# Performance work log

Measured on AMD Instinct MI355X. Metric: run time of the kernel, lower is better.

Reference implementation:

```python
import jax, jax.numpy as jnp
import numpy as np

# Dims and constants
B, DIN, H = 32768, 256, 256
STEPS = 3                 # ode_steps (>1 -> RK2 branch)
DT = 1.0 / STEPS
TAU_MIN = 0.2
ALPHA = 0.1               # plastic (hebb) mixing coefficient
ETA = 0.1                 # hebb learning rate
DECAY = 0.99              # hebb trace decay
MOE_WEIGHT = 1.0


def setup_inputs() -> dict:
    key = jax.random.key(0)
    ks = jax.random.split(key, 8)
    s = 0.02
    return {
        "x": jax.random.normal(ks[0], (B, DIN), dtype=jnp.float32),
        "h": jax.random.normal(ks[1], (B, H), dtype=jnp.float32),
        "hebb_ih": jnp.zeros((DIN, H), dtype=jnp.float32),
        "hebb_hh": jnp.zeros((H, H), dtype=jnp.float32),
        # PlasticSynapse base weights (torch Linear layout [out, in])
        "W_ih": jax.random.normal(ks[2], (H, DIN), dtype=jnp.float32) * s,
        "b_ih": jnp.zeros((H,), dtype=jnp.float32),
        "W_hh": jax.random.normal(ks[3], (H, H), dtype=jnp.float32) * s,
        "b_hh": jnp.zeros((H,), dtype=jnp.float32),
        # tau_net: Linear(DIN+H -> H) -> SiLU -> Linear(H -> H) -> Softplus
        "W_t1": jax.random.normal(ks[4], (H, DIN + H), dtype=jnp.float32) * s,
        "b_t1": jnp.zeros((H,), dtype=jnp.float32),
        "W_t2": jax.random.normal(ks[5], (H, H), dtype=jnp.float32) * s,
        "b_t2": jnp.zeros((H,), dtype=jnp.float32),
    }


def reference(x, h, hebb_ih, hebb_hh, W_ih, b_ih, W_hh, b_hh, W_t1, b_t1, W_t2, b_t2):
    bsz = x.shape[0]
    step_moe = MOE_WEIGHT / STEPS

    def syn(inp, W, b, hebb):
        # PlasticSynapse: fixed weight + alpha-scaled Hebbian trace
        return inp @ (W.T + ALPHA * hebb) + b

    def tau_net(hh):
        z = jnp.concatenate([x, hh], axis=-1)          # [B, DIN+H]
        u = z @ W_t1.T + b_t1
        u = u * jax.nn.sigmoid(u)                      # SiLU
        return jax.nn.softplus(u @ W_t2.T + b_t2) + TAU_MIN

    def dynamics(hh, heb_ih, heb_hh):
        interaction = jnp.tanh(syn(x, W_ih, b_ih, heb_ih) + syn(hh, W_hh, b_hh, heb_hh))
        return (-hh + interaction) / tau_net(hh)

    def update_hebb(hebb, pre, post):
        # decayed trace + batch-mean outer product, scaled by per-step moe weight
        return DECAY * hebb + (ETA * step_moe / bsz) * (pre.T @ post)

    # RK2 loop (steps = 3, fixed) with mid-point Hebbian updates, per original forward
    for _ in range(STEPS):
        k1 = dynamics(h, hebb_ih, hebb_hh)
        h_mid = h + 0.5 * DT * k1
        hebb_ih = update_hebb(hebb_ih, x, h_mid)
        hebb_hh = update_hebb(hebb_hh, h_mid, h_mid)
        k2 = dynamics(h_mid, hebb_ih, hebb_hh)
        h = h + DT * k2
    return h
```

## Files before the change

kernel.cpp:

```cpp
#include <hip/hip_runtime.h>
#include <stdint.h>

typedef unsigned short u16;
typedef short v8s __attribute__((ext_vector_type(8)));
typedef short v4s __attribute__((ext_vector_type(4)));
typedef float v4f __attribute__((ext_vector_type(4)));

#define NB 32768
#define ND 256
#define DTF (1.0f/3.0f)
#define ALPHA 0.1f
#define DECAY 0.99f
#define TAU_MIN 0.2f
#define HEBB_SCALE (0.1f*(1.0f/3.0f)/32768.0f)

__device__ __forceinline__ float b2f(u16 h){ return __uint_as_float(((unsigned)h)<<16); }
__device__ __forceinline__ u16 f2b(float f){
  unsigned u = __float_as_uint(f);
  u += 0x7FFFu + ((u>>16)&1u);
  return (u16)(u>>16);
}

__global__ void k_copy(const float* __restrict__ x, const float* __restrict__ h,
                       u16* __restrict__ x_bf, float* __restrict__ h_state){
  const long tot = (long)NB*ND/4;
  for (long i = blockIdx.x*(long)blockDim.x + threadIdx.x; i < tot;
       i += (long)gridDim.x*blockDim.x){
    v4f xv = *(const v4f*)(x + 4*i);
    u16 t4[4];
#pragma unroll
    for (int e=0;e<4;++e) t4[e] = f2b(xv[e]);
    *(v4s*)(x_bf + 4*i) = *(v4s*)t4;
    *(v4f*)(h_state + 4*i) = *(const v4f*)(h + 4*i);
  }
}

__global__ void k_transpose_x(const float* __restrict__ x, u16* __restrict__ xT){
  __shared__ u16 ld[64*65];
  int bt = blockIdx.x >> 2, it = blockIdx.x & 3;
  long b0 = (long)bt*64; int i0 = it*64;
  int t = threadIdx.x;
#pragma unroll
  for (int e=0;e<16;++e){
    int idx = e*256 + t; int r = idx>>6, c = idx&63;
    ld[c + r*65] = f2b(x[(b0+r)*ND + i0 + c]);
  }
  __syncthreads();
#pragma unroll
  for (int e=0;e<16;++e){
    int idx = e*256 + t; int rr = idx>>6, cc = idx&63;
    xT[(long)(i0+rr)*NB + b0 + cc] = ld[cc*65 + rr];
  }
}

__global__ void k_prep_w(const float* __restrict__ W_ih, const float* __restrict__ W_hh,
                         const float* __restrict__ W_t1, const float* __restrict__ W_t2,
                         const float* __restrict__ hebb_ih, const float* __restrict__ hebb_hh,
                         u16* __restrict__ weff_ih, u16* __restrict__ weff_hh,
                         u16* __restrict__ wt1a, u16* __restrict__ wt1b, u16* __restrict__ wt2){
  int i = blockIdx.x*blockDim.x + threadIdx.x;
  if (i >= ND*ND) return;
  int n = i >> 8, k = i & 255;
  weff_ih[i] = f2b(W_ih[i] + ALPHA*hebb_ih[k*ND + n]);
  weff_hh[i] = f2b(W_hh[i] + ALPHA*hebb_hh[k*ND + n]);
  wt1a[i] = f2b(W_t1[n*512 + k]);
  wt1b[i] = f2b(W_t1[n*512 + 256 + k]);
  wt2[i]  = f2b(W_t2[i]);
}

__launch_bounds__(512,2)
__global__ void k_gemmP(const u16* __restrict__ x_bf, const u16* __restrict__ wt1a,
                        const float* __restrict__ b_t1, u16* __restrict__ P){
  __shared__ u16 lA[128*40];
  __shared__ u16 lB[256*40];
  int t = threadIdx.x, lid = t&63, wid = t>>6, wm = wid>>2, wn = wid&3, lr = lid&15, lg = lid>>4;
  long row0 = (long)blockIdx.x*128;
  v4f z = {0.f,0.f,0.f,0.f};
  v4f acc[4][4];
#pragma unroll
  for (int a=0;a<4;++a)
#pragma unroll
    for (int b=0;b<4;++b) acc[a][b] = z;
  for (int c=0; c<8; ++c){
    __syncthreads();
    { int r=t>>2, sg=t&3;
      *(v8s*)&lA[r*40+sg*8] = *(const v8s*)(x_bf + (row0+r)*ND + c*32 + sg*8); }
#pragma unroll
    for (int it2=0; it2<2; ++it2){
      int s2=t+it2*512; int n=s2>>2, sg=s2&3;
      *(v8s*)&lB[n*40+sg*8] = *(const v8s*)(wt1a + n*ND + c*32 + sg*8);
    }
    __syncthreads();
    v8s a[4], b[4];
#pragma unroll
    for (int mf=0;mf<4;++mf) a[mf] = *(v8s*)&lA[(wm*64+mf*16+lr)*40 + lg*8];
#pragma unroll
    for (int nf=0;nf<4;++nf) b[nf] = *(v8s*)&lB[(wn*64+nf*16+lr)*40 + lg*8];
#pragma unroll
    for (int mf=0;mf<4;++mf)
#pragma unroll
      for (int nf=0;nf<4;++nf)
        acc[mf][nf] = __builtin_amdgcn_mfma_f32_16x16x32_bf16(a[mf], b[nf], acc[mf][nf], 0,0,0);
  }
#pragma unroll
  for (int mf=0;mf<4;++mf)
#pragma unroll
    for (int nf=0;nf<4;++nf)
#pragma unroll
      for (int r=0;r<4;++r){
        int rr = wm*64+mf*16+lg*4+r, cc = wn*64+nf*16+lr;
        P[(row0+rr)*ND + cc] = f2b(acc[mf][nf][r] + b_t1[cc]);
      }
}

__launch_bounds__(512,2)
__global__ void k_dyn(const u16* __restrict__ x_bf, const float* __restrict__ evalF,
                      const float* __restrict__ baseF,
                      const u16* __restrict__ weff_ih, const u16* __restrict__ weff_hh,
                      const u16* __restrict__ wt1b, const u16* __restrict__ wt2,
                      const u16* __restrict__ P,
                      const float* __restrict__ b_ih, const float* __restrict__ b_hh,
                      const float* __restrict__ b_t2,
                      float coef, float* __restrict__ outF, u16* __restrict__ outT, int writeT){
  __shared__ u16 lA[128*40];
  __shared__ u16 lB[256*40];
  __shared__ u16 lU[35840];
  __shared__ float sb1[256];
  __shared__ float sb2[256];
  int t = threadIdx.x, lid = t&63, wid = t>>6, wm = wid>>2, wn = wid&3, lr = lid&15, lg = lid>>4;
  long row0 = (long)blockIdx.x*128;
  if (t < 256){ sb1[t] = b_ih[t] + b_hh[t]; sb2[t] = b_t2[t]; }
  v4f z = {0.f,0.f,0.f,0.f};
  v4f accI[4][4], acc2[4][4];
#pragma unroll
  for (int a=0;a<4;++a)
#pragma unroll
    for (int b=0;b<4;++b){ accI[a][b] = z; acc2[a][b] = z; }

  for (int c=0; c<16; ++c){
    __syncthreads();
    { int r=t>>2, sg=t&3;
      if (c < 8){
        *(v8s*)&lA[r*40+sg*8] = *(const v8s*)(x_bf + (row0+r)*ND + c*32 + sg*8);
      } else {
        const float* s = evalF + (row0+r)*ND + (c-8)*32 + sg*8;
        v4f v0 = *(const v4f*)s, v1 = *(const v4f*)(s+4);
        u16 tmp[8];
#pragma unroll
        for (int e=0;e<4;++e){ tmp[e]=f2b(v0[e]); tmp[4+e]=f2b(v1[e]); }
        *(v8s*)&lA[r*40+sg*8] = *(v8s*)tmp;
      }
    }
    const u16* W = (c<8) ? weff_ih : weff_hh;
    int ck = (c & 7)*32;
#pragma unroll
    for (int it2=0; it2<2; ++it2){
      int s2=t+it2*512; int n=s2>>2, sg=s2&3;
      *(v8s*)&lB[n*40+sg*8] = *(const v8s*)(W + n*ND + ck + sg*8);
    }
    __syncthreads();
    v8s a[4], b[4];
#pragma unroll
    for (int mf=0;mf<4;++mf) a[mf] = *(v8s*)&lA[(wm*64+mf*16+lr)*40 + lg*8];
#pragma unroll
    for (int nf=0;nf<4;++nf) b[nf] = *(v8s*)&lB[(wn*64+nf*16+lr)*40 + lg*8];
#pragma unroll
    for (int mf=0;mf<4;++mf)
#pragma unroll
      for (int nf=0;nf<4;++nf)
        accI[mf][nf] = __builtin_amdgcn_mfma_f32_16x16x32_bf16(a[mf], b[nf], accI[mf][nf], 0,0,0);
  }

  for (int c=0; c<8; ++c){
    __syncthreads();
    { int r=t>>2, sg=t&3;
      const float* s = evalF + (row0+r)*ND + c*32 + sg*8;
      v4f v0 = *(const v4f*)s, v1 = *(const v4f*)(s+4);
      u16 tmp[8];
#pragma unroll
      for (int e=0;e<4;++e){ tmp[e]=f2b(v0[e]); tmp[4+e]=f2b(v1[e]); }
      *(v8s*)&lA[r*40+sg*8] = *(v8s*)tmp;
    }
#pragma unroll
    for (int it2=0; it2<2; ++it2){
      int s2=t+it2*512; int n=s2>>2, sg=s2&3;
      *(v8s*)&lB[n*40+sg*8] = *(const v8s*)(wt1b + n*ND + c*32 + sg*8);
    }
    __syncthreads();
    v8s a[4], b[4];
#pragma unroll
    for (int mf=0;mf<4;++mf) a[mf] = *(v8s*)&lA[(wm*64+mf*16+lr)*40 + lg*8];
#pragma unroll
    for (int nf=0;nf<4;++nf) b[nf] = *(v8s*)&lB[(wn*64+nf*16+lr)*40 + lg*8];
#pragma unroll
    for (int mf=0;mf<4;++mf)
#pragma unroll
      for (int nf=0;nf<4;++nf)
        acc2[mf][nf] = __builtin_amdgcn_mfma_f32_16x16x32_bf16(a[mf], b[nf], acc2[mf][nf], 0,0,0);
  }

#pragma unroll
  for (int mf=0;mf<4;++mf)
#pragma unroll
    for (int nf=0;nf<4;++nf)
#pragma unroll
      for (int r=0;r<4;++r){
        int rr = wm*64+mf*16+lg*4+r, cc = wn*64+nf*16+lr;
        float v = acc2[mf][nf][r] + b2f(P[(row0+rr)*ND + cc]);
        float sgm = 1.f/(1.f + __expf(-v));
        lU[rr*280 + cc] = f2b(v*sgm);
      }

  v4f acc4[4][4];
#pragma unroll
  for (int a=0;a<4;++a)
#pragma unroll
    for (int b=0;b<4;++b) acc4[a][b] = z;
  for (int c=0; c<8; ++c){
    __syncthreads();
#pragma unroll
    for (int it2=0; it2<2; ++it2){
      int s2=t+it2*512; int n=s2>>2, sg=s2&3;
      *(v8s*)&lB[n*40+sg*8] = *(const v8s*)(wt2 + n*ND + c*32 + sg*8);
    }
    __syncthreads();
    v8s a[4], b[4];
#pragma unroll
    for (int mf=0;mf<4;++mf) a[mf] = *(v8s*)&lU[(wm*64+mf*16+lr)*280 + c*32 + lg*8];
#pragma unroll
    for (int nf=0;nf<4;++nf) b[nf] = *(v8s*)&lB[(wn*64+nf*16+lr)*40 + lg*8];
#pragma unroll
    for (int mf=0;mf<4;++mf)
#pragma unroll
      for (int nf=0;nf<4;++nf)
        acc4[mf][nf] = __builtin_amdgcn_mfma_f32_16x16x32_bf16(a[mf], b[nf], acc4[mf][nf], 0,0,0);
  }

  __syncthreads();
#pragma unroll
  for (int mf=0;mf<4;++mf)
#pragma unroll
    for (int nf=0;nf<4;++nf)
#pragma unroll
      for (int r=0;r<4;++r){
        int rr = wm*64+mf*16+lg*4+r, cc = wn*64+nf*16+lr;
        long gi = (row0+rr)*ND + cc;
        float pre = accI[mf][nf][r] + sb1[cc];
        float pc = fminf(fmaxf(pre, -15.f), 15.f);
        float e2 = __expf(2.f*pc);
        float inter = (e2 - 1.f)/(e2 + 1.f);
        float zz = acc4[mf][nf][r] + sb2[cc];
        float sp = (zz > 15.f) ? zz : __logf(1.f + __expf(zz));
        float tau = sp + TAU_MIN;
        float ev = evalF[gi];
        float o = baseF[gi] + coef*(inter - ev)/tau;
        outF[gi] = o;
        if (writeT) lU[cc*136 + rr] = f2b(o);
      }
  if (writeT){
    __syncthreads();
    int cc = t>>1, r0 = (t&1)*64;
#pragma unroll
    for (int e=0;e<8;++e){
      v8s v = *(v8s*)&lU[cc*136 + r0 + e*8];
      *(v8s*)(outT + (long)cc*NB + row0 + r0 + e*8) = v;
    }
  }
}

__launch_bounds__(512,2)
__global__ void k_hebb_part(const u16* __restrict__ xT, const u16* __restrict__ hmT,
                            u16* __restrict__ part){
  __shared__ u16 lA[256*40];
  __shared__ u16 lB[256*40];
  int t = threadIdx.x, lid = t&63, wid = t>>6, wm = wid>>2, wn = wid&3, lr = lid&15, lg = lid>>4;
  int mat = blockIdx.x & 1, chunk = blockIdx.x >> 1;
  const u16* Asrc = mat ? hmT : xT;
  v4f z = {0.f,0.f,0.f,0.f};
  v4f acc[8][4];
#pragma unroll
  for (int a=0;a<8;++a)
#pragma unroll
    for (int b=0;b<4;++b) acc[a][b] = z;
  for (int kc=0; kc<8; ++kc){
    long b0 = (long)chunk*256 + kc*32;
    __syncthreads();
#pragma unroll
    for (int it2=0; it2<2; ++it2){
      int s = t + it2*512; int rr = s>>2, sg = s&3;
      *(v8s*)&lA[rr*40+sg*8] = *(const v8s*)(Asrc + (long)rr*NB + b0 + sg*8);
      *(v8s*)&lB[rr*40+sg*8] = *(const v8s*)(hmT  + (long)rr*NB + b0 + sg*8);
    }
    __syncthreads();
    v8s a[8], b[4];
#pragma unroll
    for (int mf=0;mf<8;++mf) a[mf] = *(v8s*)&lA[(wm*128+mf*16+lr)*40 + lg*8];
#pragma unroll
    for (int nf=0;nf<4;++nf) b[nf] = *(v8s*)&lB[(wn*64+nf*16+lr)*40 + lg*8];
#pragma unroll
    for (int mf=0;mf<8;++mf)
#pragma unroll
      for (int nf=0;nf<4;++nf)
        acc[mf][nf] = __builtin_amdgcn_mfma_f32_16x16x32_bf16(a[mf], b[nf], acc[mf][nf], 0,0,0);
  }
  u16* dst = part + (long)blockIdx.x*65536;
#pragma unroll
  for (int mf=0;mf<8;++mf)
#pragma unroll
    for (int nf=0;nf<4;++nf)
#pragma unroll
      for (int r=0;r<4;++r){
        int i = wm*128+mf*16+lg*4+r, j = wn*64+nf*16+lr;
        dst[i*ND + j] = f2b(acc[mf][nf][r]);
      }
}

__global__ void k_hebb_reduce(const u16* __restrict__ part,
                              const float* __restrict__ prev_ih, const float* __restrict__ prev_hh,
                              float* __restrict__ next_ih, float* __restrict__ next_hh,
                              const float* __restrict__ W_ih, const float* __restrict__ W_hh,
                              u16* __restrict__ weff_ih, u16* __restrict__ weff_hh){
  int tid = blockIdx.x*blockDim.x + threadIdx.x;
  if (tid >= 2*ND*ND) return;
  int mat = tid >> 16;
  int rem = tid & 65535;
  float s = 0.f;
  for (int c=0; c<128; ++c) s += b2f(part[(long)((c<<1)+mat)*65536 + rem]);
  const float* prev = mat ? prev_hh : prev_ih;
  float nv = DECAY*prev[rem] + HEBB_SCALE*s;
  if (mat) next_hh[rem] = nv; else next_ih[rem] = nv;
  int k = rem >> 8, n = rem & 255;
  const float* Wb = mat ? W_hh : W_ih;
  u16 wv = f2b(Wb[n*ND + k] + ALPHA*nv);
  if (mat) weff_hh[n*ND + k] = wv; else weff_ih[n*ND + k] = wv;
}

extern "C" void kernel_launch(void* const* d_in, const int* in_sizes, int n_in,
                              void* d_out, int out_size, void* d_ws, size_t ws_size,
                              hipStream_t stream) {
  const float* x       = (const float*)d_in[0];
  const float* h       = (const float*)d_in[1];
  const float* hebb_ih = (const float*)d_in[2];
  const float* hebb_hh = (const float*)d_in[3];
  const float* W_ih    = (const float*)d_in[4];
  const float* b_ih    = (const float*)d_in[5];
  const float* W_hh    = (const float*)d_in[6];
  const float* b_hh    = (const float*)d_in[7];
  const float* W_t1    = (const float*)d_in[8];
  const float* b_t1    = (const float*)d_in[9];
  const float* W_t2    = (const float*)d_in[10];
  const float* b_t2    = (const float*)d_in[11];
  float* h_state = (float*)d_out;

  char* w = (char*)d_ws;
  u16* x_bf = (u16*)w;  w += 16777216;
  u16* xT   = (u16*)w;  w += 16777216;
  u16* P    = (u16*)w;  w += 16777216;
  u16* hmT  = (u16*)w;  w += 16777216;
  float* hmF = (float*)w; w += 33554432;
  u16* part = (u16*)w;  w += 33554432;
  float* hebA_ih = (float*)w; w += 262144;
  float* hebA_hh = (float*)w; w += 262144;
  float* hebB_ih = (float*)w; w += 262144;
  float* hebB_hh = (float*)w; w += 262144;
  u16* weff_ih = (u16*)w; w += 131072;
  u16* weff_hh = (u16*)w; w += 131072;
  u16* wt1a    = (u16*)w; w += 131072;
  u16* wt1b    = (u16*)w; w += 131072;
  u16* wt2     = (u16*)w; w += 131072;
  if ((size_t)(w - (char*)d_ws) > ws_size) return;

  k_copy<<<2048,256,0,stream>>>(x, h, x_bf, h_state);
  k_transpose_x<<<2048,256,0,stream>>>(x, xT);
  k_prep_w<<<256,256,0,stream>>>(W_ih,W_hh,W_t1,W_t2,hebb_ih,hebb_hh,
                                 weff_ih,weff_hh,wt1a,wt1b,wt2);
  k_gemmP<<<256,512,0,stream>>>(x_bf, wt1a, b_t1, P);

  const float* pih = hebb_ih; const float* phh = hebb_hh;
  for (int s=0; s<3; ++s){
    float* nih = (s&1) ? hebB_ih : hebA_ih;
    float* nhh = (s&1) ? hebB_hh : hebA_hh;
    k_dyn<<<256,512,0,stream>>>(x_bf, h_state, h_state, weff_ih, weff_hh, wt1b, wt2, P,
                                b_ih, b_hh, b_t2, 0.5f*DTF, hmF, hmT, 1);
    k_hebb_part<<<256,512,0,stream>>>(xT, hmT, part);
    k_hebb_reduce<<<512,256,0,stream>>>(part, pih, phh, nih, nhh, W_ih, W_hh, weff_ih, weff_hh);
    k_dyn<<<256,512,0,stream>>>(x_bf, hmF, h_state, weff_ih, weff_hh, wt1b, wt2, P,
                                b_ih, b_hh, b_t2, DTF, h_state, (u16*)0, 0);
    pih = nih; phh = nhh;
  }
}
```

Baseline: 630.0 us.

## Pipeline dynamics kernel with async LDS loads, bf16 state, smaller tiles

Rewrites the dynamics kernel into a single 32-step unrolled MFMA loop over 64-row tiles. It uses a 5-deep ring of direct global-to-LDS async loads with XOR swizzling and hand-placed vmcnt waits, so memory fetches overlap compute. The evolving state is now kept in bf16 side buffers, so the kernel reads bf16 operands and drops the per-chunk fp32 conversion. The midpoint fp32 buffer is dropped entirely, with its base value read back from bf16. The Hebbian partial kernel uses half as many chunks, which halves the reduction work. The risks are extra rounding error from the bf16 midpoint and fragile hand-tuned wait counts.

Result: slower. 711.6 us (+13.0%).

```diff
diff --git a/kernel.cpp b/kernel.cpp
--- a/kernel.cpp
+++ b/kernel.cpp
@@ -21,17 +21,37 @@
   return (u16)(u>>16);
 }
 
+__device__ __forceinline__ void async16(const void* g, void* l){
+  __builtin_amdgcn_global_load_lds((const __attribute__((address_space(1))) unsigned*)g,
+                                   (__attribute__((address_space(3))) unsigned*)l, 16, 0, 0);
+}
+
+__device__ __forceinline__ void waitv(int n){
+  switch(n){
+    case 9: asm volatile("s_waitcnt vmcnt(9)" ::: "memory"); break;
+    case 8: asm volatile("s_waitcnt vmcnt(8)" ::: "memory"); break;
+    case 7: asm volatile("s_waitcnt vmcnt(7)" ::: "memory"); break;
+    case 6: asm volatile("s_waitcnt vmcnt(6)" ::: "memory"); break;
+    case 4: asm volatile("s_waitcnt vmcnt(4)" ::: "memory"); break;
+    case 2: asm volatile("s_waitcnt vmcnt(2)" ::: "memory"); break;
+    default: asm volatile("s_waitcnt vmcnt(0)" ::: "memory"); break;
+  }
+}
+
 __global__ void k_copy(const float* __restrict__ x, const float* __restrict__ h,
-                       u16* __restrict__ x_bf, float* __restrict__ h_state){
+                       u16* __restrict__ x_bf, u16* __restrict__ h_bf,
+                       float* __restrict__ h_state){
   const long tot = (long)NB*ND/4;
   for (long i = blockIdx.x*(long)blockDim.x + threadIdx.x; i < tot;
        i += (long)gridDim.x*blockDim.x){
     v4f xv = *(const v4f*)(x + 4*i);
-    u16 t4[4];
-#pragma unroll
-    for (int e=0;e<4;++e) t4[e] = f2b(xv[e]);
+    v4f hv = *(const v4f*)(h + 4*i);
+    u16 t4[4], t5[4];
+#pragma unroll
+    for (int e=0;e<4;++e){ t4[e] = f2b(xv[e]); t5[e] = f2b(hv[e]); }
     *(v4s*)(x_bf + 4*i) = *(v4s*)t4;
-    *(v4f*)(h_state + 4*i) = *(const v4f*)(h + 4*i);
+    *(v4s*)(h_bf + 4*i) = *(v4s*)t5;
+    *(v4f*)(h_state + 4*i) = hv;
   }
 }
 
@@ -113,137 +133,150 @@
       }
 }
 
+template<int BASEF, int WF, int WT>
 __launch_bounds__(512,2)
-__global__ void k_dyn(const u16* __restrict__ x_bf, const float* __restrict__ evalF,
-                      const float* __restrict__ baseF,
-                      const u16* __restrict__ weff_ih, const u16* __restrict__ weff_hh,
-                      const u16* __restrict__ wt1b, const u16* __restrict__ wt2,
-                      const u16* __restrict__ P,
-                      const float* __restrict__ b_ih, const float* __restrict__ b_hh,
-                      const float* __restrict__ b_t2,
-                      float coef, float* __restrict__ outF, u16* __restrict__ outT, int writeT){
-  __shared__ u16 lA[128*40];
-  __shared__ u16 lB[256*40];
-  __shared__ u16 lU[35840];
-  __shared__ float sb1[256];
-  __shared__ float sb2[256];
-  int t = threadIdx.x, lid = t&63, wid = t>>6, wm = wid>>2, wn = wid&3, lr = lid&15, lg = lid>>4;
-  long row0 = (long)blockIdx.x*128;
+__global__ void k_dyn2(const u16* __restrict__ x_bf, const u16* __restrict__ ev_bf,
+                       const float* __restrict__ baseF,
+                       const u16* __restrict__ weff_ih, const u16* __restrict__ weff_hh,
+                       const u16* __restrict__ wt1b, const u16* __restrict__ wt2,
+                       const u16* __restrict__ P,
+                       const float* __restrict__ b_ih, const float* __restrict__ b_hh,
+                       const float* __restrict__ b_t2, float coef,
+                       float* __restrict__ outF, u16* __restrict__ outB, u16* __restrict__ outT){
+  __shared__ u16 lA[5*64*32];
+  __shared__ u16 lB[5*256*32];
+  __shared__ u16 lU[64*296];
+  __shared__ float sb1[256], sb2[256];
+  const int t = threadIdx.x, lid = t&63, wid = t>>6;
+  const int wm = wid>>2, wn = wid&3, lr = lid&15, lg = lid>>4;
+  const long row0 = (long)blockIdx.x*64;
+
   if (t < 256){ sb1[t] = b_ih[t] + b_hh[t]; sb2[t] = b_t2[t]; }
+
+  const int rA  = (wid&3)*16 + (lid>>2);
+  const int scA = (lid&3) ^ ((rA>>1)&3);
+  const long aoffg = (row0 + rA)*ND + scA*8;
+  const int rB0 = wid*32 + (lid>>2), rB1 = rB0 + 16;
+  const int boffg0 = rB0*ND + (((lid&3) ^ ((rB0>>1)&3))*8);
+  const int boffg1 = rB1*ND + (((lid&3) ^ ((rB1>>1)&3))*8);
+
+  int aoff[2], boff[4], uoffb[2];
+#pragma unroll
+  for (int mf=0;mf<2;++mf){
+    int R = wm*32 + mf*16 + lr;
+    aoff[mf] = R*32 + ((lg ^ ((R>>1)&3))*8);
+    uoffb[mf] = R*296 + lg*8;
+  }
+#pragma unroll
+  for (int nf=0;nf<4;++nf){
+    int N = wn*64 + nf*16 + lr;
+    boff[nf] = N*32 + ((lg ^ ((N>>1)&3))*8);
+  }
+
+  u16 Pv[32];
+#pragma unroll
+  for (int mf=0;mf<2;++mf)
+#pragma unroll
+    for (int nf=0;nf<4;++nf)
+#pragma unroll
+      for (int r=0;r<4;++r){
+        int rr = wm*32+mf*16+lg*4+r, cc = wn*64+nf*16+lr;
+        Pv[(mf*4+nf)*4+r] = P[(row0+rr)*ND + cc];
+      }
+
+  auto stageA = [&](int jj){
+    if (wid < 4){
+      const u16* src = (jj < 8) ? ev_bf : (jj < 16 ? x_bf : ev_bf);
+      async16(src + aoffg + (jj&7)*32, lA + (jj%5)*2048 + (wid&3)*512);
+    }
+  };
+  auto stageB = [&](int jj){
+    const u16* W = (jj<8) ? wt1b : (jj<16 ? weff_ih : (jj<24 ? weff_hh : wt2));
+    int c = (jj&7)*32;
+    async16(W + c + boffg0, lB + (jj%5)*8192 + wid*1024);
+    async16(W + c + boffg1, lB + (jj%5)*8192 + wid*1024 + 512);
+  };
+
+  stageB(0); stageA(0);
+  stageB(1); stageA(1);
+  stageB(2); stageA(2);
+  stageB(3); stageA(3);
+  __syncthreads();
+
   v4f z = {0.f,0.f,0.f,0.f};
-  v4f accI[4][4], acc2[4][4];
-#pragma unroll
-  for (int a=0;a<4;++a)
-#pragma unroll
-    for (int b=0;b<4;++b){ accI[a][b] = z; acc2[a][b] = z; }
-
-  for (int c=0; c<16; ++c){
-    __syncthreads();
-    { int r=t>>2, sg=t&3;
-      if (c < 8){
-        *(v8s*)&lA[r*40+sg*8] = *(const v8s*)(x_bf + (row0+r)*ND + c*32 + sg*8);
+  v4f acc2[2][4], accI[2][4], acc4[2][4];
+#pragma unroll
+  for (int a=0;a<2;++a)
+#pragma unroll
+    for (int b=0;b<4;++b){ acc2[a][b]=z; accI[a][b]=z; acc4[a][b]=z; }
+
+#pragma unroll
+  for (int j=0; j<32; ++j){
+    int n;
+    if (wid < 4) n = (j<=20)?9:((j==21)?8:((j==22)?7:((j<=28)?6:((j==29)?4:((j==30)?2:0)))));
+    else         n = (j<=28)?6:((j==29)?4:((j==30)?2:0));
+    waitv(n);
+    __builtin_amdgcn_s_barrier();
+    if (j <= 19) stageA(j+4);
+    if (j <= 27) stageB(j+4);
+
+    v8s b[4];
+#pragma unroll
+    for (int nf=0;nf<4;++nf) b[nf] = *(v8s*)&lB[(j%5)*8192 + boff[nf]];
+
+    if (j < 24){
+      v8s a[2];
+#pragma unroll
+      for (int mf=0;mf<2;++mf) a[mf] = *(v8s*)&lA[(j%5)*2048 + aoff[mf]];
+      if (j < 8){
+#pragma unroll
+        for (int mf=0;mf<2;++mf)
+#pragma unroll
+          for (int nf=0;nf<4;++nf)
+            acc2[mf][nf] = __builtin_amdgcn_mfma_f32_16x16x32_bf16(a[mf], b[nf], acc2[mf][nf], 0,0,0);
       } else {
-        const float* s = evalF + (row0+r)*ND + (c-8)*32 + sg*8;
-        v4f v0 = *(const v4f*)s, v1 = *(const v4f*)(s+4);
-        u16 tmp[8];
-#pragma unroll
-        for (int e=0;e<4;++e){ tmp[e]=f2b(v0[e]); tmp[4+e]=f2b(v1[e]); }
-        *(v8s*)&lA[r*40+sg*8] = *(v8s*)tmp;
+#pragma unroll
+        for (int mf=0;mf<2;++mf)
+#pragma unroll
+          for (int nf=0;nf<4;++nf)
+            accI[mf][nf] = __builtin_amdgcn_mfma_f32_16x16x32_bf16(a[mf], b[nf], accI[mf][nf], 0,0,0);
       }
-    }
-    const u16* W = (c<8) ? weff_ih : weff_hh;
-    int ck = (c & 7)*32;
-#pragma unroll
-    for (int it2=0; it2<2; ++it2){
-      int s2=t+it2*512; int n=s2>>2, sg=s2&3;
-      *(v8s*)&lB[n*40+sg*8] = *(const v8s*)(W + n*ND + ck + sg*8);
-    }
-    __syncthreads();
-    v8s a[4], b[4];
-#pragma unroll
-    for (int mf=0;mf<4;++mf) a[mf] = *(v8s*)&lA[(wm*64+mf*16+lr)*40 + lg*8];
-#pragma unroll
-    for (int nf=0;nf<4;++nf) b[nf] = *(v8s*)&lB[(wn*64+nf*16+lr)*40 + lg*8];
-#pragma unroll
-    for (int mf=0;mf<4;++mf)
-#pragma unroll
-      for (int nf=0;nf<4;++nf)
-        accI[mf][nf] = __builtin_amdgcn_mfma_f32_16x16x32_bf16(a[mf], b[nf], accI[mf][nf], 0,0,0);
-  }
-
-  for (int c=0; c<8; ++c){
-    __syncthreads();
-    { int r=t>>2, sg=t&3;
-      const float* s = evalF + (row0+r)*ND + c*32 + sg*8;
-      v4f v0 = *(const v4f*)s, v1 = *(const v4f*)(s+4);
-      u16 tmp[8];
-#pragma unroll
-      for (int e=0;e<4;++e){ tmp[e]=f2b(v0[e]); tmp[4+e]=f2b(v1[e]); }
-      *(v8s*)&lA[r*40+sg*8] = *(v8s*)tmp;
-    }
-#pragma unroll
-    for (int it2=0; it2<2; ++it2){
-      int s2=t+it2*512; int n=s2>>2, sg=s2&3;
-      *(v8s*)&lB[n*40+sg*8] = *(const v8s*)(wt1b + n*ND + c*32 + sg*8);
-    }
-    __syncthreads();
-    v8s a[4], b[4];
-#pragma unroll
-    for (int mf=0;mf<4;++mf) a[mf] = *(v8s*)&lA[(wm*64+mf*16+lr)*40 + lg*8];
-#pragma unroll
-    for (int nf=0;nf<4;++nf) b[nf] = *(v8s*)&lB[(wn*64+nf*16+lr)*40 + lg*8];
-#pragma unroll
-    for (int mf=0;mf<4;++mf)
-#pragma unroll
-      for (int nf=0;nf<4;++nf)
-        acc2[mf][nf] = __builtin_amdgcn_mfma_f32_16x16x32_bf16(a[mf], b[nf], acc2[mf][nf], 0,0,0);
-  }
-
-#pragma unroll
-  for (int mf=0;mf<4;++mf)
+    } else {
+      v8s a[2];
+#pragma unroll
+      for (int mf=0;mf<2;++mf) a[mf] = *(v8s*)&lU[uoffb[mf] + (j-24)*32];
+#pragma unroll
+      for (int mf=0;mf<2;++mf)
+#pragma unroll
+        for (int nf=0;nf<4;++nf)
+          acc4[mf][nf] = __builtin_amdgcn_mfma_f32_16x16x32_bf16(a[mf], b[nf], acc4[mf][nf], 0,0,0);
+    }
+
+    if (j == 7){
+#pragma unroll
+      for (int mf=0;mf<2;++mf)
+#pragma unroll
+        for (int nf=0;nf<4;++nf)
+#pragma unroll
+          for (int r=0;r<4;++r){
+            int rr = wm*32+mf*16+lg*4+r, cc = wn*64+nf*16+lr;
+            float v = acc2[mf][nf][r] + b2f(Pv[(mf*4+nf)*4+r]);
+            float sgm = 1.f/(1.f + __expf(-v));
+            lU[rr*296 + cc] = f2b(v*sgm);
+          }
+      asm volatile("s_waitcnt lgkmcnt(0)" ::: "memory");
+    }
+  }
+
+  __syncthreads();
+
+#pragma unroll
+  for (int mf=0;mf<2;++mf)
 #pragma unroll
     for (int nf=0;nf<4;++nf)
 #pragma unroll
       for (int r=0;r<4;++r){
-        int rr = wm*64+mf*16+lg*4+r, cc = wn*64+nf*16+lr;
-        float v = acc2[mf][nf][r] + b2f(P[(row0+rr)*ND + cc]);
-        float sgm = 1.f/(1.f + __expf(-v));
-        lU[rr*280 + cc] = f2b(v*sgm);
-      }
-
-  v4f acc4[4][4];
-#pragma unroll
-  for (int a=0;a<4;++a)
-#pragma unroll
-    for (int b=0;b<4;++b) acc4[a][b] = z;
-  for (int c=0; c<8; ++c){
-    __syncthreads();
-#pragma unroll
-    for (int it2=0; it2<2; ++it2){
-      int s2=t+it2*512; int n=s2>>2, sg=s2&3;
-      *(v8s*)&lB[n*40+sg*8] = *(const v8s*)(wt2 + n*ND + c*32 + sg*8);
-    }
-    __syncthreads();
-    v8s a[4], b[4];
-#pragma unroll
-    for (int mf=0;mf<4;++mf) a[mf] = *(v8s*)&lU[(wm*64+mf*16+lr)*280 + c*32 + lg*8];
-#pragma unroll
-    for (int nf=0;nf<4;++nf) b[nf] = *(v8s*)&lB[(wn*64+nf*16+lr)*40 + lg*8];
-#pragma unroll
-    for (int mf=0;mf<4;++mf)
-#pragma unroll
-      for (int nf=0;nf<4;++nf)
-        acc4[mf][nf] = __builtin_amdgcn_mfma_f32_16x16x32_bf16(a[mf], b[nf], acc4[mf][nf], 0,0,0);
-  }
-
-  __syncthreads();
-#pragma unroll
-  for (int mf=0;mf<4;++mf)
-#pragma unroll
-    for (int nf=0;nf<4;++nf)
-#pragma unroll
-      for (int r=0;r<4;++r){
-        int rr = wm*64+mf*16+lg*4+r, cc = wn*64+nf*16+lr;
+        int rr = wm*32+mf*16+lg*4+r, cc = wn*64+nf*16+lr;
         long gi = (row0+rr)*ND + cc;
         float pre = accI[mf][nf][r] + sb1[cc];
         float pc = fminf(fmaxf(pre, -15.f), 15.f);
@@ -252,17 +285,20 @@
         float zz = acc4[mf][nf][r] + sb2[cc];
         float sp = (zz > 15.f) ? zz : __logf(1.f + __expf(zz));
         float tau = sp + TAU_MIN;
-        float ev = evalF[gi];
-        float o = baseF[gi] + coef*(inter - ev)/tau;
-        outF[gi] = o;
-        if (writeT) lU[cc*136 + rr] = f2b(o);
+        float bv, ev;
+        if (BASEF){ bv = baseF[gi]; ev = b2f(ev_bf[gi]); }
+        else      { bv = b2f(ev_bf[gi]); ev = bv; }
+        float o = bv + coef*(inter - ev)/tau;
+        if (WF) outF[gi] = o;
+        outB[gi] = f2b(o);
+        if (WT) lU[cc*72 + rr] = f2b(o);
       }
-  if (writeT){
+  if (WT){
     __syncthreads();
-    int cc = t>>1, r0 = (t&1)*64;
-#pragma unroll
-    for (int e=0;e<8;++e){
-      v8s v = *(v8s*)&lU[cc*136 + r0 + e*8];
+    int cc = t>>1, r0 = (t&1)*32;
+#pragma unroll
+    for (int e=0;e<4;++e){
+      v8s v = *(v8s*)&lU[cc*72 + r0 + e*8];
       *(v8s*)(outT + (long)cc*NB + row0 + r0 + e*8) = v;
     }
   }
@@ -282,8 +318,8 @@
   for (int a=0;a<8;++a)
 #pragma unroll
     for (int b=0;b<4;++b) acc[a][b] = z;
-  for (int kc=0; kc<8; ++kc){
-    long b0 = (long)chunk*256 + kc*32;
+  for (int kc=0; kc<16; ++kc){
+    long b0 = (long)chunk*512 + kc*32;
     __syncthreads();
 #pragma unroll
     for (int it2=0; it2<2; ++it2){
@@ -325,7 +361,7 @@
   int mat = tid >> 16;
   int rem = tid & 65535;
   float s = 0.f;
-  for (int c=0; c<128; ++c) s += b2f(part[(long)((c<<1)+mat)*65536 + rem]);
+  for (int c=0; c<64; ++c) s += b2f(part[(long)((c<<1)+mat)*65536 + rem]);
   const float* prev = mat ? prev_hh : prev_ih;
   float nv = DECAY*prev[rem] + HEBB_SCALE*s;
   if (mat) next_hh[rem] = nv; else next_ih[rem] = nv;
@@ -353,12 +389,13 @@
   float* h_state = (float*)d_out;
 
   char* w = (char*)d_ws;
-  u16* x_bf = (u16*)w;  w += 16777216;
-  u16* xT   = (u16*)w;  w += 16777216;
-  u16* P    = (u16*)w;  w += 16777216;
-  u16* hmT  = (u16*)w;  w += 16777216;
-  float* hmF = (float*)w; w += 33554432;
-  u16* part = (u16*)w;  w += 33554432;
+  u16* x_bf  = (u16*)w;  w += 16777216;
+  u16* xT    = (u16*)w;  w += 16777216;
+  u16* P     = (u16*)w;  w += 16777216;
+  u16* hmT   = (u16*)w;  w += 16777216;
+  u16* h_bf  = (u16*)w;  w += 16777216;
+  u16* hm_bf = (u16*)w;  w += 16777216;
+  u16* part  = (u16*)w;  w += 16777216;
   float* hebA_ih = (float*)w; w += 262144;
   float* hebA_hh = (float*)w; w += 262144;
   float* hebB_ih = (float*)w; w += 262144;
@@ -370,7 +407,7 @@
   u16* wt2     = (u16*)w; w += 131072;
   if ((size_t)(w - (char*)d_ws) > ws_size) return;
 
-  k_copy<<<2048,256,0,stream>>>(x, h, x_bf, h_state);
+  k_copy<<<2048,256,0,stream>>>(x, h, x_bf, h_bf, h_state);
   k_transpose_x<<<2048,256,0,stream>>>(x, xT);
   k_prep_w<<<256,256,0,stream>>>(W_ih,W_hh,W_t1,W_t2,hebb_ih,hebb_hh,
                                  weff_ih,weff_hh,wt1a,wt1b,wt2);
@@ -380,12 +417,14 @@
   for (int s=0; s<3; ++s){
     float* nih = (s&1) ? hebB_ih : hebA_ih;
     float* nhh = (s&1) ? hebB_hh : hebA_hh;
-    k_dyn<<<256,512,0,stream>>>(x_bf, h_state, h_state, weff_ih, weff_hh, wt1b, wt2, P,
-                                b_ih, b_hh, b_t2, 0.5f*DTF, hmF, hmT, 1);
-    k_hebb_part<<<256,512,0,stream>>>(xT, hmT, part);
+    k_dyn2<0,0,1><<<512,512,0,stream>>>(x_bf, h_bf, h_state, weff_ih, weff_hh, wt1b, wt2, P,
+                                        b_ih, b_hh, b_t2, 0.5f*DTF,
+                                        (float*)0, hm_bf, hmT);
+    k_hebb_part<<<128,512,0,stream>>>(xT, hmT, part);
     k_hebb_reduce<<<512,256,0,stream>>>(part, pih, phh, nih, nhh, W_ih, W_hh, weff_ih, weff_hh);
-    k_dyn<<<256,512,0,stream>>>(x_bf, hmF, h_state, weff_ih, weff_hh, wt1b, wt2, P,
-                                b_ih, b_hh, b_t2, DTF, h_state, (u16*)0, 0);
+    k_dyn2<1,1,0><<<512,512,0,stream>>>(x_bf, hm_bf, h_state, weff_ih, weff_hh, wt1b, wt2, P,
+                                        b_ih, b_hh, b_t2, DTF,
+                                        h_state, h_bf, (u16*)0);
     pih = nih; phh = nhh;
   }
 }
```
